# Optimization experiments

Measured on AMD Instinct MI355X. Metric: run time of the kernel, lower is better.

The kernel has to match this reference:

```python
import jax, jax.numpy as jnp
import numpy as np

BS = 16          # batch size (self.bs)
N = 2048         # nodes per graph
F_OUT = 40       # out_features
F_EXT = 12       # in_xfeatures
ALPHA = 0.2      # LeakyReLU negative slope
NEG = -9.0e15    # masking value from the original code


def setup_inputs() -> dict:
    key = jax.random.key(0)
    k_x, k_adj, k_ext, k_side, k_W, k_a = jax.random.split(key, 6)
    x = jax.random.normal(k_x, (BS * N, 1), dtype=jnp.float32)
    adj = (jax.random.uniform(k_adj, (N, N)) < 0.05).astype(jnp.float32)
    adj = jnp.maximum(adj, jnp.eye(N, dtype=jnp.float32))
    ext_input = jax.random.normal(k_ext, (BS * N, F_EXT), dtype=jnp.float32)
    side_input = jax.random.normal(k_side, (BS * N, 1), dtype=jnp.float32)
    # xavier_uniform with gain=1.414
    gain = 1.414
    lim_W = gain * np.sqrt(6.0 / (1 + F_OUT))
    W = jax.random.uniform(k_W, (1, F_OUT), minval=-lim_W, maxval=lim_W, dtype=jnp.float32)
    lim_a = gain * np.sqrt(6.0 / (2 * F_OUT + 1))
    a = jax.random.uniform(k_a, (2 * F_OUT, 1), minval=-lim_a, maxval=lim_a, dtype=jnp.float32)
    return {"x": x, "adj": adj, "ext_input": ext_input, "side_input": side_input, "W": W, "a": a}


def reference(x, adj, ext_input, side_input, W, a):
    # h = (input viewed as [bs, N, 1]) @ W  ->  [bs, N, F]
    h = x.reshape(BS, N, 1) @ W
    # Pairwise score e[b,i,j] = leakyrelu([h_i || h_j] @ a) = leakyrelu(h_i@a1 + h_j@a2)
    # (same math as the repeat/cat/view formulation, without the N^2*2F intermediate)
    a1 = a[:F_OUT, 0]   # [F]
    a2 = a[F_OUT:, 0]   # [F]
    f_i = h @ a1        # [bs, N]
    f_j = h @ a2        # [bs, N]
    e = jax.nn.leaky_relu(f_i[:, :, None] + f_j[:, None, :], negative_slope=ALPHA)  # [bs, N, N]
    # mask by adjacency, then (as in the original) also mask non-positive scores
    att = jnp.where(adj[None, :, :] > 0, e, NEG)
    att = jnp.where(att > 0, att, NEG)
    att = jax.nn.softmax(att, axis=2)   # dropout disabled (eval mode)
    h_prime = att @ h                    # [bs, N, F]
    return jax.nn.elu(h_prime)           # concat=True -> ELU
```

## Files before the change

kernel.cpp:

```cpp
#include <hip/hip_runtime.h>
#include <hip/hip_bf16.h>
#include <cstdint>

#define N 2048
#define BS 16
#define F_OUT 40
#define MAXDEG 256
#define LOG2E 1.44269504088896340736f

__global__ __launch_bounds__(256) void k_fused(const float* __restrict__ x,
                                               const float* __restrict__ adj,
                                               const float* __restrict__ W,
                                               const float* __restrict__ a,
                                               float* __restrict__ out) {
    const int i = blockIdx.x;
    const int t = threadIdx.x;
    const int wv = t >> 6, lane = t & 63;

    __shared__ unsigned short list[MAXDEG];
    __shared__ int wcnt[4];
    __shared__ int s_cnt;
    __shared__ float s_s1, s_s2;

    const float4* arow = reinterpret_cast<const float4*>(adj + (size_t)i * N);
    float4 v0 = arow[wv * 128 + lane];
    float4 v1 = arow[wv * 128 + 64 + lane];

    if (wv == 0) {
        float p1 = 0.f, p2 = 0.f;
        if (lane < F_OUT) {
            const float w = W[lane];
            p1 = w * a[lane];
            p2 = w * a[F_OUT + lane];
        }
        #pragma unroll
        for (int off = 32; off; off >>= 1) {
            p1 += __shfl_xor(p1, off);
            p2 += __shfl_xor(p2, off);
        }
        if (lane == 0) { s_s1 = p1 * LOG2E; s_s2 = p2 * LOG2E; }
    }

    unsigned long long m[2][4];
    int cnt = 0;
    m[0][0] = __ballot(v0.x > 0.f);
    m[0][1] = __ballot(v0.y > 0.f);
    m[0][2] = __ballot(v0.z > 0.f);
    m[0][3] = __ballot(v0.w > 0.f);
    m[1][0] = __ballot(v1.x > 0.f);
    m[1][1] = __ballot(v1.y > 0.f);
    m[1][2] = __ballot(v1.z > 0.f);
    m[1][3] = __ballot(v1.w > 0.f);
    #pragma unroll
    for (int it = 0; it < 2; ++it)
        cnt += __popcll(m[it][0]) + __popcll(m[it][1]) +
               __popcll(m[it][2]) + __popcll(m[it][3]);
    if (lane == 0) wcnt[wv] = cnt;
    __syncthreads();

    int base = 0;
    for (int u = 0; u < wv; ++u) base += wcnt[u];
    const unsigned long long lt = (1ull << lane) - 1ull;
    #pragma unroll
    for (int it = 0; it < 2; ++it) {
        const int f4idx = wv * 128 + it * 64 + lane;
        #pragma unroll
        for (int k = 0; k < 4; ++k) {
            const unsigned long long mask = m[it][k];
            if ((mask >> lane) & 1ull) {
                const int pos = base + __popcll(mask & lt);
                if (pos < MAXDEG)
                    list[pos] = (unsigned short)(f4idx * 4 + k);
            }
            base += __popcll(mask);
        }
    }
    if (t == 0) {
        int tot = wcnt[0] + wcnt[1] + wcnt[2] + wcnt[3];
        s_cnt = tot < MAXDEG ? tot : MAXDEG;
    }
    __syncthreads();

    const int deg = s_cnt;
    const float s1 = s_s1, s2 = s_s2;
    const float wl = (lane < F_OUT) ? W[lane] : 0.f;

    #pragma unroll
    for (int bb = 0; bb < 4; ++bb) {
        const int b = wv + bb * 4;
        const float* __restrict__ xb = x + b * N;
        const float zi2 = s1 * xb[i];

        float d = 0.f, ws = 0.f;
        for (int tt = lane; tt < deg; tt += 64) {
            const int jn = list[tt];
            const float xj = xb[jn];
            const float z2 = fmaf(s2, xj, zi2);
            const float e = (z2 > 0.f) ? exp2f(z2) : 0.f;
            d += e;
            ws = fmaf(e, xj, ws);
        }
        #pragma unroll
        for (int off = 32; off; off >>= 1) {
            d += __shfl_xor(d, off);
            ws += __shfl_xor(ws, off);
        }

        float p;
        if (d > 0.f) {
            p = ws / d;
        } else {
            float s = 0.f;
            for (int k = lane; k < N; k += 64) s += xb[k];
            #pragma unroll
            for (int off = 32; off; off >>= 1) s += __shfl_xor(s, off);
            p = s * (1.0f / N);
        }

        if (lane < F_OUT) {
            const float v = p * wl;
            out[((size_t)(b * N + i)) * F_OUT + lane] =
                (v > 0.f) ? v : expm1f(v);
        }
    }
}

extern "C" void kernel_launch(void* const* d_in, const int* in_sizes, int n_in,
                              void* d_out, int out_size, void* d_ws, size_t ws_size,
                              hipStream_t stream) {
    const float* x   = (const float*)d_in[0];
    const float* adj = (const float*)d_in[1];
    const float* W   = (const float*)d_in[4];
    const float* a   = (const float*)d_in[5];
    float* out = (float*)d_out;

    k_fused<<<N, 256, 0, stream>>>(x, adj, W, a, out);
}
```

Baseline: 16.09 us.

## Transpose x to node-major layout in a prep kernel and batch-vectorize gathers

Adds a prep kernel that transposes x into an [N][BS] layout, precomputes the attention scalars and the per-batch mean of x used as the fallback. The main kernel then maps 16 lanes to the 16 batches, so each neighbor gather reads 64 contiguous bytes instead of 16 scattered loads, and the lanes cover different neighbor indices in parallel. Partial sums are reduced through shared memory, and all 640 outputs are written in one cooperative loop. The cost is a second kernel launch, a workspace round trip and extra synchronisation.

```diff
diff --git a/kernel.cpp b/kernel.cpp
--- a/kernel.cpp
+++ b/kernel.cpp
@@ -8,41 +8,73 @@
 #define MAXDEG 256
 #define LOG2E 1.44269504088896340736f
 
-__global__ __launch_bounds__(256) void k_fused(const float* __restrict__ x,
-                                               const float* __restrict__ adj,
-                                               const float* __restrict__ W,
-                                               const float* __restrict__ a,
-                                               float* __restrict__ out) {
-    const int i = blockIdx.x;
+
+__global__ __launch_bounds__(256) void k_prep(const float* __restrict__ x,
+                                              const float* __restrict__ W,
+                                              const float* __restrict__ a,
+                                              float* __restrict__ xT,
+                                              float* __restrict__ scal) {
+    const int b = blockIdx.x;
     const int t = threadIdx.x;
-    const int wv = t >> 6, lane = t & 63;
+    const float4* xb4 = reinterpret_cast<const float4*>(x + (size_t)b * N);
+    float s = 0.f;
+    #pragma unroll
+    for (int it = 0; it < N / (256 * 4); ++it) {
+        const int k4 = t + it * 256;
+        const float4 v = xb4[k4];
+        const int k = k4 * 4;
+        xT[(k + 0) * BS + b] = v.x;
+        xT[(k + 1) * BS + b] = v.y;
+        xT[(k + 2) * BS + b] = v.z;
+        xT[(k + 3) * BS + b] = v.w;
+        s += v.x + v.y + v.z + v.w;
+    }
+    __shared__ float sd[256];
+    sd[t] = s; __syncthreads();
+    for (int off = 128; off; off >>= 1) {
+        if (t < off) sd[t] += sd[t + off];
+        __syncthreads();
+    }
+    if (t == 0) scal[2 + b] = sd[0] * (1.0f / N);
 
-    __shared__ unsigned short list[MAXDEG];
-    __shared__ int wcnt[4];
-    __shared__ int s_cnt;
-    __shared__ float s_s1, s_s2;
-
-    const float4* arow = reinterpret_cast<const float4*>(adj + (size_t)i * N);
-    float4 v0 = arow[wv * 128 + lane];
-    float4 v1 = arow[wv * 128 + 64 + lane];
-
-    if (wv == 0) {
+    if (b == 0 && t < 64) {
         float p1 = 0.f, p2 = 0.f;
-        if (lane < F_OUT) {
-            const float w = W[lane];
-            p1 = w * a[lane];
-            p2 = w * a[F_OUT + lane];
+        if (t < F_OUT) {
+            const float w = W[t];
+            p1 = w * a[t];
+            p2 = w * a[F_OUT + t];
         }
         #pragma unroll
         for (int off = 32; off; off >>= 1) {
             p1 += __shfl_xor(p1, off);
             p2 += __shfl_xor(p2, off);
         }
-        if (lane == 0) { s_s1 = p1 * LOG2E; s_s2 = p2 * LOG2E; }
+        if (t == 0) { scal[0] = p1 * LOG2E; scal[1] = p2 * LOG2E; }
     }
+}
+
+__global__ __launch_bounds__(256) void k_main(const float* __restrict__ adj,
+                                              const float* __restrict__ xT,
+                                              const float* __restrict__ scal,
+                                              const float* __restrict__ W,
+                                              float* __restrict__ out) {
+    const int i = blockIdx.x;
+    const int t = threadIdx.x;
+    const int wv = t >> 6, lane = t & 63;
+    const int b16 = lane & 15;
+    const int ng  = lane >> 4;
+
+    __shared__ unsigned short list[MAXDEG];
+    __shared__ int wcnt[4];
+    __shared__ int s_cnt;
+    __shared__ float sdd[4][16], sdw[4][16];
+    __shared__ float p16[16];
+
+    const float4* arow = reinterpret_cast<const float4*>(adj + (size_t)i * N);
+    float4 v0 = arow[wv * 128 + lane];
+    float4 v1 = arow[wv * 128 + 64 + lane];
 
     unsigned long long m[2][4];
-    int cnt = 0;
     m[0][0] = __ballot(v0.x > 0.f);
     m[0][1] = __ballot(v0.y > 0.f);
     m[0][2] = __ballot(v0.z > 0.f);
@@ -51,6 +83,7 @@
     m[1][1] = __ballot(v1.y > 0.f);
     m[1][2] = __ballot(v1.z > 0.f);
     m[1][3] = __ballot(v1.w > 0.f);
+    int cnt = 0;
     #pragma unroll
     for (int it = 0; it < 2; ++it)
         cnt += __popcll(m[it][0]) + __popcll(m[it][1]) +
@@ -76,52 +109,42 @@
         }
     }
     if (t == 0) {
-        int tot = wcnt[0] + wcnt[1] + wcnt[2] + wcnt[3];
+        const int tot = wcnt[0] + wcnt[1] + wcnt[2] + wcnt[3];
         s_cnt = tot < MAXDEG ? tot : MAXDEG;
     }
     __syncthreads();
 
     const int deg = s_cnt;
-    const float s1 = s_s1, s2 = s_s2;
-    const float wl = (lane < F_OUT) ? W[lane] : 0.f;
+    const float s1 = scal[0], s2 = scal[1];
+    const float xiv = xT[i * BS + b16];
+    const float zi2 = s1 * xiv;
 
-    #pragma unroll
-    for (int bb = 0; bb < 4; ++bb) {
-        const int b = wv + bb * 4;
-        const float* __restrict__ xb = x + b * N;
-        const float zi2 = s1 * xb[i];
+    float d = 0.f, w = 0.f;
+    for (int idx = wv * 4 + ng; idx < deg; idx += 16) {
+        const int jn = list[idx];
+        const float xj = xT[jn * BS + b16];
+        const float z2 = fmaf(s2, xj, zi2);
+        const float e = (z2 > 0.f) ? exp2f(z2) : 0.f;
+        d += e;
+        w = fmaf(e, xj, w);
+    }
+    d += __shfl_xor(d, 16); d += __shfl_xor(d, 32);
+    w += __shfl_xor(w, 16); w += __shfl_xor(w, 32);
+    if (lane < 16) { sdd[wv][lane] = d; sdw[wv][lane] = w; }
+    __syncthreads();
 
-        float d = 0.f, ws = 0.f;
-        for (int tt = lane; tt < deg; tt += 64) {
-            const int jn = list[tt];
-            const float xj = xb[jn];
-            const float z2 = fmaf(s2, xj, zi2);
-            const float e = (z2 > 0.f) ? exp2f(z2) : 0.f;
-            d += e;
-            ws = fmaf(e, xj, ws);
-        }
-        #pragma unroll
-        for (int off = 32; off; off >>= 1) {
-            d += __shfl_xor(d, off);
-            ws += __shfl_xor(ws, off);
-        }
+    if (t < BS) {
+        const float dt = sdd[0][t] + sdd[1][t] + sdd[2][t] + sdd[3][t];
+        const float wt = sdw[0][t] + sdw[1][t] + sdw[2][t] + sdw[3][t];
+        p16[t] = (dt > 0.f) ? (wt / dt) : scal[2 + t];
+    }
+    __syncthreads();
 
-        float p;
-        if (d > 0.f) {
-            p = ws / d;
-        } else {
-            float s = 0.f;
-            for (int k = lane; k < N; k += 64) s += xb[k];
-            #pragma unroll
-            for (int off = 32; off; off >>= 1) s += __shfl_xor(s, off);
-            p = s * (1.0f / N);
-        }
-
-        if (lane < F_OUT) {
-            const float v = p * wl;
-            out[((size_t)(b * N + i)) * F_OUT + lane] =
-                (v > 0.f) ? v : expm1f(v);
-        }
+    for (int idx = t; idx < BS * F_OUT; idx += 256) {
+        const int b = idx / F_OUT;
+        const int f = idx - b * F_OUT;
+        const float v = p16[b] * W[f];
+        out[((size_t)(b * N + i)) * F_OUT + f] = (v > 0.f) ? v : expm1f(v);
     }
 }
 
@@ -134,5 +157,10 @@
     const float* a   = (const float*)d_in[5];
     float* out = (float*)d_out;
 
-    k_fused<<<N, 256, 0, stream>>>(x, adj, W, a, out);
+    char* ws = (char*)d_ws;
+    float* xT   = (float*)ws;
+    float* scal = (float*)(ws + (size_t)N * BS * sizeof(float));
+
+    k_prep<<<BS, 256, 0, stream>>>(x, W, a, xT, scal);
+    k_main<<<N, 256, 0, stream>>>(adj, xT, scal, W, out);
 }
```

Result: slower. 17.73 us (+10.2%).
